# Kernel optimization log

Hardware: AMD Instinct MI355X
Metric: run time of the kernel (lower is better)

## Reference

```python
import jax, jax.numpy as jnp
import numpy as np
from jax import lax

T = 8  # hardcoded temporal length in the torch module

def _dwconv_t(z, w, b):
    # z: (N, C, T, 1); w: (C, 1, k, 1) depthwise; 'same' padding along T
    k = w.shape[2]
    p = (k - 1) // 2
    out = lax.conv_general_dilated(
        z, w, window_strides=(1, 1), padding=[(p, p), (0, 0)],
        feature_group_count=z.shape[1],
        dimension_numbers=('NCHW', 'OIHW', 'NCHW'))
    return out + b[None, :, None, None]


def setup_inputs() -> dict:
    key = jax.random.key(0)
    ks = jax.random.split(key, 13)
    C, IC, H, W, B = 1024, 512, 14, 14, 16
    s = lambda k, shp, scale: jax.random.normal(k, shp, dtype=jnp.float32) * scale
    return {
        'x':   s(ks[0], (B * T, C, H, W), 1.0),
        'w1':  s(ks[1], (IC, C, 1, 1), 0.03),
        'b1':  s(ks[2], (IC,), 0.02),
        'wb1': s(ks[3], (IC, 1, 1, 1), 0.3),
        'bb1': s(ks[4], (IC,), 0.02),
        'wb2': s(ks[5], (IC, 1, 3, 1), 0.3),
        'bb2': s(ks[6], (IC,), 0.02),
        'wb3': s(ks[7], (IC, 1, 5, 1), 0.3),
        'bb3': s(ks[8], (IC,), 0.02),
        'wb4': s(ks[9], (IC, 1, 7, 1), 0.3),
        'bb4': s(ks[10], (IC,), 0.02),
        'w2':  s(ks[11], (C, IC, 1, 1), 0.03),
        'b2':  s(ks[12], (C,), 0.02),
    }


def reference(x, w1, b1, wb1, bb1, wb2, bb2, wb3, bb3, wb4, bb4, w2, b2):
    BT, C, H, W = x.shape
    B = BT // T
    IC = w1.shape[0]
    # conv1: 1x1 pointwise conv == channel GEMM
    y = jnp.einsum('nchw,oc->nohw', x, w1[:, :, 0, 0]) + b1[None, :, None, None]
    # (B*T, IC, H, W) -> (B, T, IC, H, W) -> (B, H, W, IC, T) -> (B*H*W, IC, T, 1)
    z = y.reshape(B, T, IC, H, W).transpose(0, 3, 4, 2, 1).reshape(B * H * W, IC, T, 1)
    out = (_dwconv_t(z, wb1, bb1) + _dwconv_t(z, wb2, bb2)
           + _dwconv_t(z, wb3, bb3) + _dwconv_t(z, wb4, bb4))
    # (B*H*W, IC, T, 1) -> (B, H, W, IC, T) -> (B, T, IC, H, W) -> (B*T, IC, H, W)
    out = out.reshape(B, H, W, IC, T).transpose(0, 4, 3, 1, 2).reshape(BT, IC, H, W)
    # conv2: 1x1 pointwise conv back to C channels
    out = jnp.einsum('nihw,oi->nohw', out, w2[:, :, 0, 0]) + b2[None, :, None, None]
    return x + out
```

## Files before the change

### kernel.cpp

```cpp
#include <hip/hip_runtime.h>
#include <hip/hip_bf16.h>

typedef short short8 __attribute__((ext_vector_type(8)));
typedef float f32x4 __attribute__((ext_vector_type(4)));
typedef unsigned int uint;

#define CB   16
#define TT   8
#define CIN  1024
#define ICH  512
#define HWS  196
#define NPB  1568
#define NF   25088

static __device__ __forceinline__ unsigned short f2bf(float f) {
  __hip_bfloat16 h = __float2bfloat16(f); unsigned short u; __builtin_memcpy(&u, &h, 2); return u;
}

static __device__ __forceinline__ void stage16(const void* g, void* l) {
  __builtin_amdgcn_global_load_lds(
      (const __attribute__((address_space(1))) unsigned int*)(unsigned long long)g,
      (__attribute__((address_space(3))) unsigned int*)(unsigned int)(unsigned long long)l,
      16, 0, 0);
}

__global__ void k_prep(const float* __restrict__ x, __hip_bfloat16* __restrict__ xbT,
    const float* __restrict__ w1, const float* __restrict__ w2,
    const float* __restrict__ wb1, const float* __restrict__ bb1,
    const float* __restrict__ wb2, const float* __restrict__ bb2,
    const float* __restrict__ wb3, const float* __restrict__ bb3,
    const float* __restrict__ wb4, const float* __restrict__ bb4,
    __hip_bfloat16* __restrict__ w1b, __hip_bfloat16* __restrict__ w2b,
    float* __restrict__ weff, float* __restrict__ beff) {
  int bid = blockIdx.x;
  if (bid >= CB * TT * 16 * 4) {
    int idx = (bid - CB * TT * 16 * 4) * 256 + threadIdx.x;
    if (idx < CIN * ICH) {
      w1b[idx] = __float2bfloat16(w1[idx]);
      w2b[idx] = __float2bfloat16(w2[idx]);
    }
    if (idx < ICH) {
      float e[7];
#pragma unroll
      for (int u = 0; u < 7; u++) e[u] = wb4[idx * 7 + u];
#pragma unroll
      for (int u = 0; u < 5; u++) e[u + 1] += wb3[idx * 5 + u];
#pragma unroll
      for (int u = 0; u < 3; u++) e[u + 2] += wb2[idx * 3 + u];
      e[3] += wb1[idx];
#pragma unroll
      for (int u = 0; u < 7; u++) weff[idx * 8 + u] = e[u];
      weff[idx * 8 + 7] = 0.f;
      beff[idx] = bb1[idx] + bb2[idx] + bb3[idx] + bb4[idx];
    }
    return;
  }
  __shared__ float tile[64][51];
  int ht = bid & 3;
  int ct = (bid >> 2) & 15;
  int t  = (bid >> 6) & 7;
  int b  = bid >> 9;
  int c0 = ct * 64, h0 = ht * 49;
  const float* src = x + ((size_t)((b * TT + t) * CIN + c0)) * HWS + h0;
  for (int idx = threadIdx.x; idx < 64 * 49; idx += 256) {
    int r = idx / 49, q = idx - r * 49;
    tile[r][q] = src[(size_t)r * HWS + q];
  }
  __syncthreads();
  for (int idx = threadIdx.x; idx < 49 * 16; idx += 256) {
    int h = idx >> 4, g = idx & 15;
    ushort4 pk;
    pk.x = f2bf(tile[g * 4 + 0][h]);
    pk.y = f2bf(tile[g * 4 + 1][h]);
    pk.z = f2bf(tile[g * 4 + 2][h]);
    pk.w = f2bf(tile[g * 4 + 3][h]);
    size_t n1 = (size_t)(h0 + h) * TT + t;
    *(ushort4*)&xbT[((size_t)b * NPB + n1) * CIN + (c0 + g * 4)] = pk;
  }
}

template <int KD>
static __device__ __forceinline__ void gemm_core64(
    const __hip_bfloat16* __restrict__ Ar,
    const __hip_bfloat16* __restrict__ Br,
    __hip_bfloat16* As, __hip_bfloat16* Bs, f32x4 (&acc)[8][4]) {
  constexpr int NT = KD / 64;
  const int tid = threadIdx.x;
  const int lane = tid & 63, w = tid >> 6;
  const int wm = w >> 2, wn = w & 3;
  const int ln = lane & 15, lm = lane >> 4;
  const int srow = lane >> 3;
  const int schk = (lane & 7) ^ srow;
  const __hip_bfloat16* aS = Ar + (size_t)(w * 16 + srow) * KD + schk * 8;
  const __hip_bfloat16* bS = Br + (size_t)(w * 16 + srow) * KD + schk * 8;
  __hip_bfloat16* aD = As + (w * 16) * 64;
  __hip_bfloat16* bD = Bs + (w * 16) * 64;
  const int ck0 = ((lm) ^ (ln & 7)) * 8;
  const int ck1 = ((4 + lm) ^ (ln & 7)) * 8;
  int ra[8], rb[4];
#pragma unroll
  for (int mf = 0; mf < 8; mf++) ra[mf] = (mf * 32 + wm * 16 + ln) * 64;
#pragma unroll
  for (int nf = 0; nf < 4; nf++) rb[nf] = (wn * 64 + nf * 16 + ln) * 64;

#define STG_(src, dst, h, q, kt, buf) \
  stage16(src + (size_t)((h) * 128 + (q) * 8) * KD + (kt) * 64, \
          dst + (buf) * 16384 + ((h) * 128 + (q) * 8) * 64)

  STG_(bS, bD, 0, 0, 0, 0); STG_(bS, bD, 0, 1, 0, 0);
  STG_(bS, bD, 1, 0, 0, 0); STG_(bS, bD, 1, 1, 0, 0);
  STG_(aS, aD, 0, 0, 0, 0); STG_(aS, aD, 0, 1, 0, 0);
  STG_(aS, aD, 1, 0, 0, 0); STG_(aS, aD, 1, 1, 0, 0);

  short8 af[4], bfA[4], bfB[4];
  for (int t = 0; t < NT; t++) {
    const int buf = t & 1, nb = buf ^ 1;
    const bool has = (t + 1 < NT);
    const int bufo = buf * 16384;
    const __hip_bfloat16* Ab = As + bufo;
    const __hip_bfloat16* Bb = Bs + bufo;
    if (has) { STG_(bS, bD, 0, 0, t + 1, nb); STG_(bS, bD, 0, 1, t + 1, nb); }
    if (has) asm volatile("s_waitcnt vmcnt(4)" ::: "memory");
    else     asm volatile("s_waitcnt vmcnt(2)" ::: "memory");
    asm volatile("s_barrier" ::: "memory");
#pragma unroll
    for (int q = 0; q < 4; q++) af[q] = *(const short8*)&Ab[ra[q] + ck0];
#pragma unroll
    for (int nf = 0; nf < 4; nf++) bfA[nf] = *(const short8*)&Bb[rb[nf] + ck0];
    asm volatile("s_waitcnt lgkmcnt(0)" ::: "memory");
    __builtin_amdgcn_sched_barrier(0);
    __builtin_amdgcn_s_setprio(1);
#pragma unroll
    for (int nf = 0; nf < 4; nf++)
#pragma unroll
      for (int q = 0; q < 4; q++)
        acc[q][nf] = __builtin_amdgcn_mfma_f32_16x16x32_bf16(af[q], bfA[nf], acc[q][nf], 0, 0, 0);
    __builtin_amdgcn_s_setprio(0);
    if (has) { STG_(bS, bD, 1, 0, t + 1, nb); STG_(bS, bD, 1, 1, t + 1, nb); }
#pragma unroll
    for (int q = 0; q < 4; q++) af[q] = *(const short8*)&Ab[ra[q] + ck1];
#pragma unroll
    for (int nf = 0; nf < 4; nf++) bfB[nf] = *(const short8*)&Bb[rb[nf] + ck1];
    asm volatile("s_waitcnt lgkmcnt(0)" ::: "memory");
    __builtin_amdgcn_sched_barrier(0);
    __builtin_amdgcn_s_setprio(1);
#pragma unroll
    for (int nf = 0; nf < 4; nf++)
#pragma unroll
      for (int q = 0; q < 4; q++)
        acc[q][nf] = __builtin_amdgcn_mfma_f32_16x16x32_bf16(af[q], bfB[nf], acc[q][nf], 0, 0, 0);
    __builtin_amdgcn_s_setprio(0);
    if (has) { STG_(aS, aD, 0, 0, t + 1, nb); STG_(aS, aD, 0, 1, t + 1, nb); }
    if (has) asm volatile("s_waitcnt vmcnt(6)" ::: "memory");
    else     asm volatile("s_waitcnt vmcnt(0)" ::: "memory");
    asm volatile("s_barrier" ::: "memory");
#pragma unroll
    for (int q = 0; q < 4; q++) af[q] = *(const short8*)&Ab[ra[4 + q] + ck0];
    asm volatile("s_waitcnt lgkmcnt(0)" ::: "memory");
    __builtin_amdgcn_sched_barrier(0);
    __builtin_amdgcn_s_setprio(1);
#pragma unroll
    for (int nf = 0; nf < 4; nf++)
#pragma unroll
      for (int q = 0; q < 4; q++)
        acc[4 + q][nf] = __builtin_amdgcn_mfma_f32_16x16x32_bf16(af[q], bfA[nf], acc[4 + q][nf], 0, 0, 0);
    __builtin_amdgcn_s_setprio(0);
    if (has) { STG_(aS, aD, 1, 0, t + 1, nb); STG_(aS, aD, 1, 1, t + 1, nb); }
#pragma unroll
    for (int q = 0; q < 4; q++) af[q] = *(const short8*)&Ab[ra[4 + q] + ck1];
    asm volatile("s_waitcnt lgkmcnt(0)" ::: "memory");
    __builtin_amdgcn_sched_barrier(0);
    __builtin_amdgcn_s_setprio(1);
#pragma unroll
    for (int nf = 0; nf < 4; nf++)
#pragma unroll
      for (int q = 0; q < 4; q++)
        acc[4 + q][nf] = __builtin_amdgcn_mfma_f32_16x16x32_bf16(af[q], bfB[nf], acc[4 + q][nf], 0, 0, 0);
    __builtin_amdgcn_s_setprio(0);
    asm volatile("s_barrier" ::: "memory");
  }
#undef STG_
}

__global__ __launch_bounds__(512, 2) void k_gemm1(const __hip_bfloat16* __restrict__ xbT,
                                                  const __hip_bfloat16* __restrict__ w1b,
                                                  const float* __restrict__ b1,
                                                  const float* __restrict__ weff,
                                                  const float* __restrict__ beff,
                                                  __hip_bfloat16* __restrict__ dwT) {
  __shared__ __hip_bfloat16 As[2 * 256 * 64];
  __shared__ __hip_bfloat16 Bs[2 * 256 * 64];
  int xcd = blockIdx.x & 7, i = blockIdx.x >> 3;
  int id = (xcd < 4 ? xcd * 25 : 100 + (xcd - 4) * 24) + i;
  int rt = id >> 1, ot = id & 1;
  int n0 = rt * 256, o0 = ot * 256;
  f32x4 acc[8][4];
#pragma unroll
  for (int a = 0; a < 8; a++)
#pragma unroll
    for (int c = 0; c < 4; c++) acc[a][c] = (f32x4){0.f, 0.f, 0.f, 0.f};
  gemm_core64<1024>(xbT + (size_t)n0 * CIN, w1b + (size_t)o0 * CIN, As, Bs, acc);

  int tid = threadIdx.x, lane = tid & 63, w = tid >> 6;
  int wm = w >> 2, wn = w & 3, ln = lane & 15, lm = lane >> 4;
  bool hiT = (lm & 1);
#pragma unroll
  for (int nf = 0; nf < 4; nf++) {
    int o = o0 + wn * 64 + nf * 16 + ln;
    float e[7];
#pragma unroll
    for (int u = 0; u < 7; u++) e[u] = weff[o * 8 + u];
    float be = beff[o];
    float bo = b1[o];
#pragma unroll
    for (int mf = 0; mf < 8; mf++) {
      float av[4], pv[4];
#pragma unroll
      for (int j = 0; j < 4; j++) av[j] = acc[mf][nf][j] + bo;
#pragma unroll
      for (int j = 0; j < 4; j++) pv[j] = __shfl_xor(av[j], 16, 64);
      float ov[4];
      if (hiT) {
#pragma unroll
        for (int j = 0; j < 4; j++) {
          float s = be;
#pragma unroll
          for (int u = 0; u < 7; u++) {
            int ss = 4 + j + u - 3;
            if (ss >= 0 && ss < 8) s += e[u] * (ss < 4 ? pv[ss] : av[ss - 4]);
          }
          ov[j] = s;
        }
      } else {
#pragma unroll
        for (int j = 0; j < 4; j++) {
          float s = be;
#pragma unroll
          for (int u = 0; u < 7; u++) {
            int ss = j + u - 3;
            if (ss >= 0 && ss < 8) s += e[u] * (ss < 4 ? av[ss] : pv[ss - 4]);
          }
          ov[j] = s;
        }
      }
      int grow = n0 + mf * 32 + wm * 16 + ((lm >> 1) & 1) * 8;
      int gidx = grow >> 3;
      int gb = gidx / HWS, ghw = gidx - gb * HWS;
      int tb = hiT ? 4 : 0;
#pragma unroll
      for (int j = 0; j < 4; j++) {
        size_t rr = (size_t)gb * NPB + (size_t)(tb + j) * HWS + ghw;
        dwT[rr * ICH + o] = __float2bfloat16(ov[j]);
      }
    }
  }
}

__global__ __launch_bounds__(512, 2) void k_gemm2(const __hip_bfloat16* __restrict__ dwT,
                                                  const __hip_bfloat16* __restrict__ w2b,
                                                  const float* __restrict__ b2,
                                                  const float* __restrict__ xres,
                                                  float* __restrict__ out) {
  __shared__ __align__(16) char smem[131072];
  __hip_bfloat16* As = (__hip_bfloat16*)smem;
  __hip_bfloat16* Bs = (__hip_bfloat16*)(smem + 65536);
  int id = (blockIdx.x & 7) * 49 + (blockIdx.x >> 3);
  int nt = id >> 2, mt = id & 3;
  int n0 = nt * 256, m0 = mt * 256;
  f32x4 acc[8][4];
#pragma unroll
  for (int a = 0; a < 8; a++)
#pragma unroll
    for (int c = 0; c < 4; c++) acc[a][c] = (f32x4){0.f, 0.f, 0.f, 0.f};
  gemm_core64<512>(w2b + (size_t)m0 * ICH, dwT + (size_t)n0 * ICH, As, Bs, acc);

  int tid = threadIdx.x, lane = tid & 63, w = tid >> 6;
  int wm = w >> 2, wn = w & 3, ln = lane & 15, lm = lane >> 4;
  float* arr = (float*)smem;
  int fc = tid & 63, fr = tid >> 6;
  int n2 = n0 + fc * 4;
  int bb = n2 / NPB, r = n2 - bb * NPB;
  int t2 = r / HWS, hw = r - t2 * HWS;
  size_t base4 = ((size_t)((bb * TT + t2) * CIN)) * HWS + hw;
#pragma unroll
  for (int p = 0; p < 4; p++) {
    __syncthreads();
#pragma unroll
    for (int q2 = 0; q2 < 2; q2++) {
      int mf = p * 2 + q2;
#pragma unroll
      for (int nf = 0; nf < 4; nf++)
#pragma unroll
        for (int j = 0; j < 4; j++)
          arr[(q2 * 32 + wm * 16 + lm * 4 + j) * 260 + wn * 64 + nf * 16 + ln] = acc[mf][nf][j];
    }
    __syncthreads();
#pragma unroll
    for (int it = 0; it < 8; it++) {
      int o2l = it * 8 + fr;
      f32x4 v = *(const f32x4*)&arr[o2l * 260 + fc * 4];
      int o2 = m0 + p * 64 + o2l;
      float bo = b2[o2];
      size_t a = base4 + (size_t)o2 * HWS;
      float4 xr = *(const float4*)(xres + a);
      float4 ov = make_float4(v[0] + bo + xr.x, v[1] + bo + xr.y,
                              v[2] + bo + xr.z, v[3] + bo + xr.w);
      *(float4*)(out + a) = ov;
    }
  }
}

extern "C" void kernel_launch(void* const* d_in, const int* in_sizes, int n_in,
                              void* d_out, int out_size, void* d_ws, size_t ws_size,
                              hipStream_t stream) {
  const float* x   = (const float*)d_in[0];
  const float* w1  = (const float*)d_in[1];
  const float* b1  = (const float*)d_in[2];
  const float* wb1 = (const float*)d_in[3];
  const float* bb1 = (const float*)d_in[4];
  const float* wb2 = (const float*)d_in[5];
  const float* bb2 = (const float*)d_in[6];
  const float* wb3 = (const float*)d_in[7];
  const float* bb3 = (const float*)d_in[8];
  const float* wb4 = (const float*)d_in[9];
  const float* bb4 = (const float*)d_in[10];
  const float* w2  = (const float*)d_in[11];
  const float* b2  = (const float*)d_in[12];
  float* out = (float*)d_out;

  __hip_bfloat16* xbT = (__hip_bfloat16*)d_out;

  char* ws = (char*)d_ws;
  __hip_bfloat16* dwT = (__hip_bfloat16*)ws;
  __hip_bfloat16* w1b = (__hip_bfloat16*)(ws + 25690112);
  __hip_bfloat16* w2b = (__hip_bfloat16*)(ws + 25690112 + 1048576);
  float* weff = (float*)(ws + 25690112 + 2097152);
  float* beff = weff + 4096;

  k_prep<<<CB * TT * 16 * 4 + (CIN * ICH + 255) / 256, 256, 0, stream>>>(
      x, xbT, w1, w2, wb1, bb1, wb2, bb2, wb3, bb3, wb4, bb4, w1b, w2b, weff, beff);
  k_gemm1<<<196, 512, 0, stream>>>(xbT, w1b, b1, weff, beff, dwT);
  k_gemm2<<<392, 512, 0, stream>>>(dwT, w2b, b2, x, out);
}
```

Measured before the change: 126.1 us.

## Double GEMM workgroups to 1024 threads with half the accumulators per wave

Both GEMM kernels now run 16 waves per 256x256 tile instead of 8. Each wave owns a 64-row slice split into four 16-row fragments instead of eight, so accumulator registers per wave are halved. Staging, waitcnt counts, the epilogue indexing and the end-of-iteration barrier placement are all rewritten to match. The aim is more waves for latency hiding, at the cost of more barrier traffic and half as much MFMA work per LDS fragment load.

```diff
diff --git a/kernel.cpp b/kernel.cpp
--- a/kernel.cpp
+++ b/kernel.cpp
@@ -80,10 +80,10 @@
 }
 
 template <int KD>
-static __device__ __forceinline__ void gemm_core64(
+static __device__ __forceinline__ void gemm_core16(
     const __hip_bfloat16* __restrict__ Ar,
     const __hip_bfloat16* __restrict__ Br,
-    __hip_bfloat16* As, __hip_bfloat16* Bs, f32x4 (&acc)[8][4]) {
+    __hip_bfloat16* As, __hip_bfloat16* Bs, f32x4 (&acc)[4][4]) {
   constexpr int NT = KD / 64;
   const int tid = threadIdx.x;
   const int lane = tid & 63, w = tid >> 6;
@@ -91,115 +91,108 @@
   const int ln = lane & 15, lm = lane >> 4;
   const int srow = lane >> 3;
   const int schk = (lane & 7) ^ srow;
-  const __hip_bfloat16* aS = Ar + (size_t)(w * 16 + srow) * KD + schk * 8;
-  const __hip_bfloat16* bS = Br + (size_t)(w * 16 + srow) * KD + schk * 8;
-  __hip_bfloat16* aD = As + (w * 16) * 64;
-  __hip_bfloat16* bD = Bs + (w * 16) * 64;
+  const __hip_bfloat16* aS = Ar + (size_t)(w * 8 + srow) * KD + schk * 8;
+  const __hip_bfloat16* bS = Br + (size_t)(w * 8 + srow) * KD + schk * 8;
+  __hip_bfloat16* aD = As + (w * 8) * 64;
+  __hip_bfloat16* bD = Bs + (w * 8) * 64;
   const int ck0 = ((lm) ^ (ln & 7)) * 8;
   const int ck1 = ((4 + lm) ^ (ln & 7)) * 8;
-  int ra[8], rb[4];
-#pragma unroll
-  for (int mf = 0; mf < 8; mf++) ra[mf] = (mf * 32 + wm * 16 + ln) * 64;
-#pragma unroll
-  for (int nf = 0; nf < 4; nf++) rb[nf] = (wn * 64 + nf * 16 + ln) * 64;
-
-#define STG_(src, dst, h, q, kt, buf) \
-  stage16(src + (size_t)((h) * 128 + (q) * 8) * KD + (kt) * 64, \
-          dst + (buf) * 16384 + ((h) * 128 + (q) * 8) * 64)
-
-  STG_(bS, bD, 0, 0, 0, 0); STG_(bS, bD, 0, 1, 0, 0);
-  STG_(bS, bD, 1, 0, 0, 0); STG_(bS, bD, 1, 1, 0, 0);
-  STG_(aS, aD, 0, 0, 0, 0); STG_(aS, aD, 0, 1, 0, 0);
-  STG_(aS, aD, 1, 0, 0, 0); STG_(aS, aD, 1, 1, 0, 0);
-
-  short8 af[4], bfA[4], bfB[4];
+  const int rab = (wm * 16 + ln) * 64;
+  const int rbb = (wn * 64 + ln) * 64;
+
+#define STG(src, dst, h, kt, buf) \
+  stage16(src + (size_t)((h) * 128) * KD + (kt) * 64, dst + (buf) * 16384 + ((h) * 128) * 64)
+
+  STG(bS, bD, 0, 0, 0); STG(bS, bD, 1, 0, 0);
+  STG(aS, aD, 0, 0, 0); STG(aS, aD, 1, 0, 0);
+
+  short8 af0, af1, bfA[4], bfB[4];
   for (int t = 0; t < NT; t++) {
     const int buf = t & 1, nb = buf ^ 1;
     const bool has = (t + 1 < NT);
-    const int bufo = buf * 16384;
-    const __hip_bfloat16* Ab = As + bufo;
-    const __hip_bfloat16* Bb = Bs + bufo;
-    if (has) { STG_(bS, bD, 0, 0, t + 1, nb); STG_(bS, bD, 0, 1, t + 1, nb); }
-    if (has) asm volatile("s_waitcnt vmcnt(4)" ::: "memory");
-    else     asm volatile("s_waitcnt vmcnt(2)" ::: "memory");
+    const __hip_bfloat16* Ab = As + buf * 16384;
+    const __hip_bfloat16* Bb = Bs + buf * 16384;
+    if (has) STG(bS, bD, 0, t + 1, nb);
+    if (has) asm volatile("s_waitcnt vmcnt(2)" ::: "memory");
+    else     asm volatile("s_waitcnt vmcnt(1)" ::: "memory");
     asm volatile("s_barrier" ::: "memory");
-#pragma unroll
-    for (int q = 0; q < 4; q++) af[q] = *(const short8*)&Ab[ra[q] + ck0];
-#pragma unroll
-    for (int nf = 0; nf < 4; nf++) bfA[nf] = *(const short8*)&Bb[rb[nf] + ck0];
+    af0 = *(const short8*)&Ab[rab + ck0];
+    af1 = *(const short8*)&Ab[rab + 4096 + ck0];
+#pragma unroll
+    for (int nf = 0; nf < 4; nf++) bfA[nf] = *(const short8*)&Bb[rbb + nf * 1024 + ck0];
     asm volatile("s_waitcnt lgkmcnt(0)" ::: "memory");
     __builtin_amdgcn_sched_barrier(0);
     __builtin_amdgcn_s_setprio(1);
 #pragma unroll
-    for (int nf = 0; nf < 4; nf++)
-#pragma unroll
-      for (int q = 0; q < 4; q++)
-        acc[q][nf] = __builtin_amdgcn_mfma_f32_16x16x32_bf16(af[q], bfA[nf], acc[q][nf], 0, 0, 0);
+    for (int nf = 0; nf < 4; nf++) {
+      acc[0][nf] = __builtin_amdgcn_mfma_f32_16x16x32_bf16(af0, bfA[nf], acc[0][nf], 0, 0, 0);
+      acc[1][nf] = __builtin_amdgcn_mfma_f32_16x16x32_bf16(af1, bfA[nf], acc[1][nf], 0, 0, 0);
+    }
     __builtin_amdgcn_s_setprio(0);
-    if (has) { STG_(bS, bD, 1, 0, t + 1, nb); STG_(bS, bD, 1, 1, t + 1, nb); }
-#pragma unroll
-    for (int q = 0; q < 4; q++) af[q] = *(const short8*)&Ab[ra[q] + ck1];
-#pragma unroll
-    for (int nf = 0; nf < 4; nf++) bfB[nf] = *(const short8*)&Bb[rb[nf] + ck1];
+    if (has) STG(bS, bD, 1, t + 1, nb);
+    af0 = *(const short8*)&Ab[rab + ck1];
+    af1 = *(const short8*)&Ab[rab + 4096 + ck1];
+#pragma unroll
+    for (int nf = 0; nf < 4; nf++) bfB[nf] = *(const short8*)&Bb[rbb + nf * 1024 + ck1];
     asm volatile("s_waitcnt lgkmcnt(0)" ::: "memory");
     __builtin_amdgcn_sched_barrier(0);
     __builtin_amdgcn_s_setprio(1);
 #pragma unroll
-    for (int nf = 0; nf < 4; nf++)
-#pragma unroll
-      for (int q = 0; q < 4; q++)
-        acc[q][nf] = __builtin_amdgcn_mfma_f32_16x16x32_bf16(af[q], bfB[nf], acc[q][nf], 0, 0, 0);
+    for (int nf = 0; nf < 4; nf++) {
+      acc[0][nf] = __builtin_amdgcn_mfma_f32_16x16x32_bf16(af0, bfB[nf], acc[0][nf], 0, 0, 0);
+      acc[1][nf] = __builtin_amdgcn_mfma_f32_16x16x32_bf16(af1, bfB[nf], acc[1][nf], 0, 0, 0);
+    }
     __builtin_amdgcn_s_setprio(0);
-    if (has) { STG_(aS, aD, 0, 0, t + 1, nb); STG_(aS, aD, 0, 1, t + 1, nb); }
-    if (has) asm volatile("s_waitcnt vmcnt(6)" ::: "memory");
+    if (has) STG(aS, aD, 0, t + 1, nb);
+    if (has) asm volatile("s_waitcnt vmcnt(3)" ::: "memory");
     else     asm volatile("s_waitcnt vmcnt(0)" ::: "memory");
     asm volatile("s_barrier" ::: "memory");
-#pragma unroll
-    for (int q = 0; q < 4; q++) af[q] = *(const short8*)&Ab[ra[4 + q] + ck0];
+    af0 = *(const short8*)&Ab[rab + 2 * 4096 + ck0];
+    af1 = *(const short8*)&Ab[rab + 3 * 4096 + ck0];
     asm volatile("s_waitcnt lgkmcnt(0)" ::: "memory");
     __builtin_amdgcn_sched_barrier(0);
     __builtin_amdgcn_s_setprio(1);
 #pragma unroll
-    for (int nf = 0; nf < 4; nf++)
-#pragma unroll
-      for (int q = 0; q < 4; q++)
-        acc[4 + q][nf] = __builtin_amdgcn_mfma_f32_16x16x32_bf16(af[q], bfA[nf], acc[4 + q][nf], 0, 0, 0);
+    for (int nf = 0; nf < 4; nf++) {
+      acc[2][nf] = __builtin_amdgcn_mfma_f32_16x16x32_bf16(af0, bfA[nf], acc[2][nf], 0, 0, 0);
+      acc[3][nf] = __builtin_amdgcn_mfma_f32_16x16x32_bf16(af1, bfA[nf], acc[3][nf], 0, 0, 0);
+    }
     __builtin_amdgcn_s_setprio(0);
-    if (has) { STG_(aS, aD, 1, 0, t + 1, nb); STG_(aS, aD, 1, 1, t + 1, nb); }
-#pragma unroll
-    for (int q = 0; q < 4; q++) af[q] = *(const short8*)&Ab[ra[4 + q] + ck1];
+    if (has) STG(aS, aD, 1, t + 1, nb);
+    af0 = *(const short8*)&Ab[rab + 2 * 4096 + ck1];
+    af1 = *(const short8*)&Ab[rab + 3 * 4096 + ck1];
     asm volatile("s_waitcnt lgkmcnt(0)" ::: "memory");
     __builtin_amdgcn_sched_barrier(0);
+    asm volatile("s_barrier" ::: "memory");
     __builtin_amdgcn_s_setprio(1);
 #pragma unroll
-    for (int nf = 0; nf < 4; nf++)
-#pragma unroll
-      for (int q = 0; q < 4; q++)
-        acc[4 + q][nf] = __builtin_amdgcn_mfma_f32_16x16x32_bf16(af[q], bfB[nf], acc[4 + q][nf], 0, 0, 0);
+    for (int nf = 0; nf < 4; nf++) {
+      acc[2][nf] = __builtin_amdgcn_mfma_f32_16x16x32_bf16(af0, bfB[nf], acc[2][nf], 0, 0, 0);
+      acc[3][nf] = __builtin_amdgcn_mfma_f32_16x16x32_bf16(af1, bfB[nf], acc[3][nf], 0, 0, 0);
+    }
     __builtin_amdgcn_s_setprio(0);
-    asm volatile("s_barrier" ::: "memory");
-  }
-#undef STG_
-}
-
-__global__ __launch_bounds__(512, 2) void k_gemm1(const __hip_bfloat16* __restrict__ xbT,
-                                                  const __hip_bfloat16* __restrict__ w1b,
-                                                  const float* __restrict__ b1,
-                                                  const float* __restrict__ weff,
-                                                  const float* __restrict__ beff,
-                                                  __hip_bfloat16* __restrict__ dwT) {
+  }
+#undef STG
+}
+
+__global__ __launch_bounds__(1024, 4) void k_gemm1(const __hip_bfloat16* __restrict__ xbT,
+                                                   const __hip_bfloat16* __restrict__ w1b,
+                                                   const float* __restrict__ b1,
+                                                   const float* __restrict__ weff,
+                                                   const float* __restrict__ beff,
+                                                   __hip_bfloat16* __restrict__ dwT) {
   __shared__ __hip_bfloat16 As[2 * 256 * 64];
   __shared__ __hip_bfloat16 Bs[2 * 256 * 64];
   int xcd = blockIdx.x & 7, i = blockIdx.x >> 3;
   int id = (xcd < 4 ? xcd * 25 : 100 + (xcd - 4) * 24) + i;
   int rt = id >> 1, ot = id & 1;
   int n0 = rt * 256, o0 = ot * 256;
-  f32x4 acc[8][4];
-#pragma unroll
-  for (int a = 0; a < 8; a++)
+  f32x4 acc[4][4];
+#pragma unroll
+  for (int a = 0; a < 4; a++)
 #pragma unroll
     for (int c = 0; c < 4; c++) acc[a][c] = (f32x4){0.f, 0.f, 0.f, 0.f};
-  gemm_core64<1024>(xbT + (size_t)n0 * CIN, w1b + (size_t)o0 * CIN, As, Bs, acc);
+  gemm_core16<1024>(xbT + (size_t)n0 * CIN, w1b + (size_t)o0 * CIN, As, Bs, acc);
 
   int tid = threadIdx.x, lane = tid & 63, w = tid >> 6;
   int wm = w >> 2, wn = w & 3, ln = lane & 15, lm = lane >> 4;
@@ -213,7 +206,7 @@
     float be = beff[o];
     float bo = b1[o];
 #pragma unroll
-    for (int mf = 0; mf < 8; mf++) {
+    for (int mf = 0; mf < 4; mf++) {
       float av[4], pv[4];
 #pragma unroll
       for (int j = 0; j < 4; j++) av[j] = acc[mf][nf][j] + bo;
@@ -243,7 +236,7 @@
           ov[j] = s;
         }
       }
-      int grow = n0 + mf * 32 + wm * 16 + ((lm >> 1) & 1) * 8;
+      int grow = n0 + mf * 64 + wm * 16 + ((lm >> 1) & 1) * 8;
       int gidx = grow >> 3;
       int gb = gidx / HWS, ghw = gidx - gb * HWS;
       int tb = hiT ? 4 : 0;
@@ -256,23 +249,23 @@
   }
 }
 
-__global__ __launch_bounds__(512, 2) void k_gemm2(const __hip_bfloat16* __restrict__ dwT,
-                                                  const __hip_bfloat16* __restrict__ w2b,
-                                                  const float* __restrict__ b2,
-                                                  const float* __restrict__ xres,
-                                                  float* __restrict__ out) {
+__global__ __launch_bounds__(1024, 4) void k_gemm2(const __hip_bfloat16* __restrict__ dwT,
+                                                   const __hip_bfloat16* __restrict__ w2b,
+                                                   const float* __restrict__ b2,
+                                                   const float* __restrict__ xres,
+                                                   float* __restrict__ out) {
   __shared__ __align__(16) char smem[131072];
   __hip_bfloat16* As = (__hip_bfloat16*)smem;
   __hip_bfloat16* Bs = (__hip_bfloat16*)(smem + 65536);
   int id = (blockIdx.x & 7) * 49 + (blockIdx.x >> 3);
   int nt = id >> 2, mt = id & 3;
   int n0 = nt * 256, m0 = mt * 256;
-  f32x4 acc[8][4];
-#pragma unroll
-  for (int a = 0; a < 8; a++)
+  f32x4 acc[4][4];
+#pragma unroll
+  for (int a = 0; a < 4; a++)
 #pragma unroll
     for (int c = 0; c < 4; c++) acc[a][c] = (f32x4){0.f, 0.f, 0.f, 0.f};
-  gemm_core64<512>(w2b + (size_t)m0 * ICH, dwT + (size_t)n0 * ICH, As, Bs, acc);
+  gemm_core16<512>(w2b + (size_t)m0 * ICH, dwT + (size_t)n0 * ICH, As, Bs, acc);
 
   int tid = threadIdx.x, lane = tid & 63, w = tid >> 6;
   int wm = w >> 2, wn = w & 3, ln = lane & 15, lm = lane >> 4;
@@ -286,18 +279,14 @@
   for (int p = 0; p < 4; p++) {
     __syncthreads();
 #pragma unroll
-    for (int q2 = 0; q2 < 2; q2++) {
-      int mf = p * 2 + q2;
-#pragma unroll
-      for (int nf = 0; nf < 4; nf++)
-#pragma unroll
-        for (int j = 0; j < 4; j++)
-          arr[(q2 * 32 + wm * 16 + lm * 4 + j) * 260 + wn * 64 + nf * 16 + ln] = acc[mf][nf][j];
-    }
+    for (int nf = 0; nf < 4; nf++)
+#pragma unroll
+      for (int j = 0; j < 4; j++)
+        arr[(wm * 16 + lm * 4 + j) * 260 + wn * 64 + nf * 16 + ln] = acc[p][nf][j];
     __syncthreads();
 #pragma unroll
-    for (int it = 0; it < 8; it++) {
-      int o2l = it * 8 + fr;
+    for (int it = 0; it < 4; it++) {
+      int o2l = it * 16 + fr;
       f32x4 v = *(const f32x4*)&arr[o2l * 260 + fc * 4];
       int o2 = m0 + p * 64 + o2l;
       float bo = b2[o2];
@@ -339,6 +328,6 @@
 
   k_prep<<<CB * TT * 16 * 4 + (CIN * ICH + 255) / 256, 256, 0, stream>>>(
       x, xbT, w1, w2, wb1, bb1, wb2, bb2, wb3, bb3, wb4, bb4, w1b, w2b, weff, beff);
-  k_gemm1<<<196, 512, 0, stream>>>(xbT, w1b, b1, weff, beff, dwT);
-  k_gemm2<<<392, 512, 0, stream>>>(dwT, w2b, b2, x, out);
-}
+  k_gemm1<<<196, 1024, 0, stream>>>(xbT, w1b, b1, weff, beff, dwT);
+  k_gemm2<<<392, 1024, 0, stream>>>(dwT, w2b, b2, x, out);
+}
```

Result: faster. 123.2 us (-2.3%).
